# Kernel tuning notes

Measured on AMD Instinct MI355X. Metric: run time of the kernel, lower is better.

Reference implementation:

```python
import jax, jax.numpy as jnp
import numpy as np

N = 100000
E = 1600000
H = 4
C = 128
F_IN = 182
D = H * C  # 512
NEG_SLOPE = 0.2
LN_EPS = 1e-5


def _p(key, shape, scale=0.05):
    return jax.random.normal(key, shape, dtype=jnp.float32) * scale


def setup_inputs() -> dict:
    key = jax.random.key(0)
    ks = jax.random.split(key, 20)
    x = jax.random.normal(ks[0], (N, F_IN), dtype=jnp.float32)
    edge_index = jax.random.randint(ks[1], (2, E), 0, N, dtype=jnp.int64)
    inp = {
        "x": x,
        "edge_index": edge_index,
        # GAT layer 1
        "W1": _p(ks[2], (F_IN, D)),
        "a_src1": _p(ks[3], (H, C)),
        "a_dst1": _p(ks[4], (H, C)),
        "b1": _p(ks[5], (D,)),
        "g1": jnp.ones((D,), jnp.float32),
        "be1": jnp.zeros((D,), jnp.float32),
        # GAT layer 2
        "W2": _p(ks[6], (D, D)),
        "a_src2": _p(ks[7], (H, C)),
        "a_dst2": _p(ks[8], (H, C)),
        "b2": _p(ks[9], (D,)),
        "g2": jnp.ones((D,), jnp.float32),
        "be2": jnp.zeros((D,), jnp.float32),
        # classifier MLP
        "Wc1": _p(ks[10], (D, D)),
        "bc1": jnp.zeros((D,), jnp.float32),
        "Wc2": _p(ks[11], (D, 2)),
        "bc2": jnp.zeros((2,), jnp.float32),
    }
    return inp


def _gat_conv(x, src, dst, W, a_src, a_dst, b):
    # x: [N, Fin] -> h: [N, H, C]
    h = (x @ W).reshape(N, H, C)
    # per-node attention contributions: [N, H]
    s_src = jnp.sum(h * a_src, axis=-1)
    s_dst = jnp.sum(h * a_dst, axis=-1)
    # per-edge raw score: [E+N, H]
    e = jax.nn.leaky_relu(s_src[src] + s_dst[dst], NEG_SLOPE)
    # segment softmax over incoming edges of each dst node
    emax = jax.ops.segment_max(e, dst, num_segments=N)
    p = jnp.exp(e - emax[dst])
    denom = jax.ops.segment_sum(p, dst, num_segments=N)
    alpha = p / denom[dst]  # [E+N, H]
    # weighted aggregation of source features: [N, H, C]
    out = jax.ops.segment_sum(alpha[:, :, None] * h[src], dst, num_segments=N)
    return out.reshape(N, D) + b


def _layer_norm(x, g, b):
    mu = jnp.mean(x, axis=-1, keepdims=True)
    var = jnp.mean(jnp.square(x - mu), axis=-1, keepdims=True)
    return (x - mu) * jax.lax.rsqrt(var + LN_EPS) * g + b


def reference(x, edge_index, W1, a_src1, a_dst1, b1, g1, be1,
              W2, a_src2, a_dst2, b2, g2, be2, Wc1, bc1, Wc2, bc2):
    # add self-loops (PyG GATConv default)
    loops = jnp.arange(N, dtype=edge_index.dtype)
    src = jnp.concatenate([edge_index[0], loops])
    dst = jnp.concatenate([edge_index[1], loops])

    h1 = _gat_conv(x, src, dst, W1, a_src1, a_dst1, b1)
    h1 = jax.nn.elu(_layer_norm(h1, g1, be1))
    h2 = _gat_conv(h1, src, dst, W2, a_src2, a_dst2, b2)
    h2 = jax.nn.elu(_layer_norm(h2, g2, be2))
    # classifier (dropout is identity in eval)
    z = jax.nn.relu(h2 @ Wc1 + bc1)
    return z @ Wc2 + bc2
```

## Files before the change

### kernel.cpp

```cpp
#include <hip/hip_runtime.h>
#include <math.h>

static constexpr int N_NODES = 100000;
static constexpr int N_EDGES = 1600000;
static constexpr int E_TOT   = N_NODES + N_EDGES;
static constexpr int D   = 512;
static constexpr int FIN = 182;
static constexpr int K1P = 192;
static constexpr int M_PAD = 100096;
static constexpr float NEG_SLOPE = 0.2f;
static constexpr float LN_EPS = 1e-5f;

typedef __attribute__((ext_vector_type(8))) short short8;
typedef __attribute__((ext_vector_type(4))) float floatx4;
typedef __attribute__((ext_vector_type(2))) float floatx2;

__device__ __forceinline__ unsigned short f2bf(float f) {
  unsigned int x = __builtin_bit_cast(unsigned int, f);
  x += 0x7fffu + ((x >> 16) & 1u);
  return (unsigned short)(x >> 16);
}
__device__ __forceinline__ void unpack2(unsigned int w, float& lo, float& hi) {
  lo = __builtin_bit_cast(float, w << 16);
  hi = __builtin_bit_cast(float, w & 0xffff0000u);
}

typedef __attribute__((address_space(1))) const void gv_t;
typedef __attribute__((address_space(3))) void lv_t;
__device__ __forceinline__ void gll16(const void* g, void* l) {
  __builtin_amdgcn_global_load_lds((gv_t*)g, (lv_t*)l, 16, 0, 0);
}

__global__ __launch_bounds__(256) void k_init(const int* __restrict__ ei,
                                              int* __restrict__ deg,
                                              int* __restrict__ counter,
                                              int* __restrict__ flag) {
  int i = blockIdx.x * 256 + threadIdx.x;
  if (i < N_NODES) deg[i] = 0;
  if (blockIdx.x == 0) {
    bool nz = false;
#pragma unroll
    for (int rp = 0; rp < 8; ++rp) {
      int j = threadIdx.x + rp * 256;
      nz |= (ei[2 * j + 1] != 0);
    }
    __shared__ int sh[4];
    int wv = threadIdx.x >> 6;
    if ((threadIdx.x & 63) == 0) sh[wv] = 0;
    __syncthreads();
    if (__any(nz) && (threadIdx.x & 63) == 0) sh[wv] = 1;
    __syncthreads();
    if (threadIdx.x == 0) {
      *flag = sh[0] | sh[1] | sh[2] | sh[3];
      *counter = 0;
    }
  }
}

__device__ __forceinline__ int edge_src(const int* ei, int f, int i) {
  return f ? ei[i] : ei[2 * i];
}
__device__ __forceinline__ int edge_dst(const int* ei, int f, int i) {
  return f ? ei[N_EDGES + i] : ei[2 * (N_EDGES + i)];
}

__global__ __launch_bounds__(256) void k_count(const int* __restrict__ ei,
                                               const int* __restrict__ flag,
                                               int* __restrict__ deg) {
  int i = blockIdx.x * 256 + threadIdx.x;
  if (i >= E_TOT) return;
  int f = *flag;
  int d = (i < N_EDGES) ? edge_dst(ei, f, i) : (i - N_EDGES);
  atomicAdd(deg + d, 1);
}

__global__ __launch_bounds__(256) void k_alloc(const int* __restrict__ deg,
                                               int* __restrict__ off,
                                               int* __restrict__ pos,
                                               int* __restrict__ counter) {
  int i = blockIdx.x * 256 + threadIdx.x;
  if (i >= N_NODES) return;
  int r = atomicAdd(counter, deg[i]);
  off[i] = r;
  pos[i] = r;
}

__global__ __launch_bounds__(256) void k_fill(const int* __restrict__ ei,
                                              const int* __restrict__ flag,
                                              int* __restrict__ pos,
                                              int* __restrict__ csr_src) {
  int i = blockIdx.x * 256 + threadIdx.x;
  if (i >= E_TOT) return;
  int f = *flag;
  int s, d;
  if (i < N_EDGES) { s = edge_src(ei, f, i); d = edge_dst(ei, f, i); }
  else             { s = d = i - N_EDGES; }
  int slot = atomicAdd(pos + d, 1);
  csr_src[slot] = s;
}

__global__ __launch_bounds__(256) void k_cvt_x(const float* __restrict__ x,
                                               unsigned short* __restrict__ xb) {
  int i = blockIdx.x * 256 + threadIdx.x;
  if (i >= N_NODES * K1P) return;
  int row = i / K1P, col = i - row * K1P;
  float v = (col < FIN) ? x[(size_t)row * FIN + col] : 0.f;
  xb[i] = f2bf(v);
}

__global__ __launch_bounds__(256) void k_cvt_wt(const float* __restrict__ W,
                                                unsigned short* __restrict__ Wt,
                                                int K, int Kpad) {
  int i = blockIdx.x * 256 + threadIdx.x;
  if (i >= 512 * Kpad) return;
  int n = i / Kpad, k = i - n * Kpad;
  Wt[i] = f2bf(k < K ? W[(size_t)k * 512 + n] : 0.f);
}

__global__ __launch_bounds__(256) void k_out_init(const float* __restrict__ bc2,
                                                  float* __restrict__ out) {
  int i = blockIdx.x * 256 + threadIdx.x;
  if (i < N_NODES) {
    float2 v; v.x = bc2[0]; v.y = bc2[1];
    ((float2*)out)[i] = v;
  }
}

__global__ __launch_bounds__(256)
void gemm_fused(const unsigned short* __restrict__ A,
                const unsigned short* __restrict__ Bt,
                const float* __restrict__ a_src,
                const float* __restrict__ a_dst,
                float2* __restrict__ ssc,
                float* __restrict__ s_dst,
                unsigned char* __restrict__ h8,
                int lda)
{
  __shared__ unsigned short As[2][128 * 32];
  __shared__ unsigned short Bs[2][128 * 32];
  const int t    = threadIdx.x;
  const int w    = t >> 6;
  const int lane = t & 63;
  const int r    = lane & 15;
  const int q    = lane >> 4;
  const int bm   = blockIdx.y * 128;
  const int bn   = blockIdx.x * 128;
  const int wm   = (w >> 1) * 64;
  const int wn   = (w & 1) * 64;

  const int ch0 = (w * 2 + 0) * 64 + lane;
  const int ch1 = (w * 2 + 1) * 64 + lane;
  const unsigned short* gA0 = A + (size_t)(bm + (ch0 >> 2)) * lda + (ch0 & 3) * 8;
  const unsigned short* gA1 = A + (size_t)(bm + (ch1 >> 2)) * lda + (ch1 & 3) * 8;
  const unsigned short* gB0 = Bt + (size_t)(bn + (ch0 >> 2)) * lda + (ch0 & 3) * 8;
  const unsigned short* gB1 = Bt + (size_t)(bn + (ch1 >> 2)) * lda + (ch1 & 3) * 8;

  floatx4 acc[4][4] = {};

  for (int k0 = 0; k0 < lda; k0 += 64) {
    gll16(gA0 + k0,      &As[0][(w * 2 + 0) * 512]);
    gll16(gA1 + k0,      &As[0][(w * 2 + 1) * 512]);
    gll16(gB0 + k0,      &Bs[0][(w * 2 + 0) * 512]);
    gll16(gB1 + k0,      &Bs[0][(w * 2 + 1) * 512]);
    gll16(gA0 + k0 + 32, &As[1][(w * 2 + 0) * 512]);
    gll16(gA1 + k0 + 32, &As[1][(w * 2 + 1) * 512]);
    gll16(gB0 + k0 + 32, &Bs[1][(w * 2 + 0) * 512]);
    gll16(gB1 + k0 + 32, &Bs[1][(w * 2 + 1) * 512]);
    __syncthreads();

#pragma unroll
    for (int half = 0; half < 2; ++half) {
      short8 af[4], bfr[4];
#pragma unroll
      for (int im = 0; im < 4; ++im)
        af[im] = *(const short8*)(&As[half][(wm + im * 16 + r) * 32 + q * 8]);
#pragma unroll
      for (int in = 0; in < 4; ++in)
        bfr[in] = *(const short8*)(&Bs[half][(wn + in * 16 + r) * 32 + q * 8]);
#pragma unroll
      for (int im = 0; im < 4; ++im)
#pragma unroll
        for (int in = 0; in < 4; ++in)
          acc[im][in] = __builtin_amdgcn_mfma_f32_16x16x32_bf16(
              af[im], bfr[in], acc[im][in], 0, 0, 0);
    }
    __syncthreads();
  }

  float* sred = (float*)&As[0][0];
  float* qscl = (float*)&Bs[0][0];

  float asv[4], adv[4];
#pragma unroll
  for (int in = 0; in < 4; ++in) {
    asv[in] = a_src[bn + wn + in * 16 + r];
    adv[in] = a_dst[bn + wn + in * 16 + r];
  }
#pragma unroll
  for (int im = 0; im < 4; ++im) {
    float ps_[4], pd_[4], pm_[4];
#pragma unroll
    for (int rr = 0; rr < 4; ++rr) {
      float s = 0.f, d = 0.f, m = 0.f;
#pragma unroll
      for (int in = 0; in < 4; ++in) {
        float v = acc[im][in][rr];
        s += v * asv[in];
        d += v * adv[in];
        m = fmaxf(m, fabsf(v));
      }
      ps_[rr] = s; pd_[rr] = d; pm_[rr] = m;
    }
#pragma unroll
    for (int o2 = 1; o2 < 16; o2 <<= 1) {
#pragma unroll
      for (int rr = 0; rr < 4; ++rr) {
        ps_[rr] += __shfl_xor(ps_[rr], o2);
        pd_[rr] += __shfl_xor(pd_[rr], o2);
        pm_[rr] = fmaxf(pm_[rr], __shfl_xor(pm_[rr], o2));
      }
    }
    if (r == 0) {
#pragma unroll
      for (int rr = 0; rr < 4; ++rr) {
        int r64 = im * 16 + q * 4 + rr;
        sred[(w * 64 + r64) * 4 + 0] = ps_[rr];
        sred[(w * 64 + r64) * 4 + 1] = pd_[rr];
        sred[(w * 64 + r64) * 4 + 2] = pm_[rr];
      }
    }
  }
  __syncthreads();

  if (t < 128) {
    int hf = t >> 6;
    int r64 = t & 63;
    const float* pa = sred + ((hf * 2 + 0) * 64 + r64) * 4;
    const float* pb = sred + ((hf * 2 + 1) * 64 + r64) * 4;
    float s  = pa[0] + pb[0];
    float dd = pa[1] + pb[1];
    float am = fmaxf(fmaxf(pa[2], pb[2]), 1e-20f);
    qscl[t] = 127.f / am;
    int node = bm + t;
    if (node < N_NODES) {
      float2 sc; sc.x = s; sc.y = am * (1.f / 127.f);
      ssc[(size_t)node * 4 + blockIdx.x] = sc;
      s_dst[(size_t)node * 4 + blockIdx.x] = dd;
    }
  }
  __syncthreads();

#pragma unroll
  for (int im = 0; im < 4; ++im) {
#pragma unroll
    for (int rr = 0; rr < 4; ++rr) {
      int lr = wm + im * 16 + q * 4 + rr;
      float qs = qscl[lr];
      unsigned int pk = 0;
#pragma unroll
      for (int in = 0; in < 4; ++in) {
        int qv = (int)rintf(acc[im][in][rr] * qs) + 128;
        pk |= (unsigned int)(qv & 255) << (8 * in);
      }
      *(unsigned int*)(h8 + (size_t)(bm + lr) * 512 + bn + wn + 4 * r) = pk;
    }
  }
}

__global__ __launch_bounds__(256)
void gemm_cls(const unsigned short* __restrict__ A,
              const unsigned short* __restrict__ Bt,
              const float* __restrict__ bc1,
              const float* __restrict__ Wc2,
              float* __restrict__ out,
              int lda)
{
  __shared__ unsigned short As[2][128 * 32];
  __shared__ unsigned short Bs[2][128 * 32];
  const int t    = threadIdx.x;
  const int w    = t >> 6;
  const int lane = t & 63;
  const int r    = lane & 15;
  const int q    = lane >> 4;
  const int bm   = blockIdx.y * 128;
  const int bn   = blockIdx.x * 128;
  const int wm   = (w >> 1) * 64;
  const int wn   = (w & 1) * 64;

  const int ch0 = (w * 2 + 0) * 64 + lane;
  const int ch1 = (w * 2 + 1) * 64 + lane;
  const unsigned short* gA0 = A + (size_t)(bm + (ch0 >> 2)) * lda + (ch0 & 3) * 8;
  const unsigned short* gA1 = A + (size_t)(bm + (ch1 >> 2)) * lda + (ch1 & 3) * 8;
  const unsigned short* gB0 = Bt + (size_t)(bn + (ch0 >> 2)) * lda + (ch0 & 3) * 8;
  const unsigned short* gB1 = Bt + (size_t)(bn + (ch1 >> 2)) * lda + (ch1 & 3) * 8;

  floatx4 acc[4][4] = {};

  for (int k0 = 0; k0 < lda; k0 += 64) {
    gll16(gA0 + k0,      &As[0][(w * 2 + 0) * 512]);
    gll16(gA1 + k0,      &As[0][(w * 2 + 1) * 512]);
    gll16(gB0 + k0,      &Bs[0][(w * 2 + 0) * 512]);
    gll16(gB1 + k0,      &Bs[0][(w * 2 + 1) * 512]);
    gll16(gA0 + k0 + 32, &As[1][(w * 2 + 0) * 512]);
    gll16(gA1 + k0 + 32, &As[1][(w * 2 + 1) * 512]);
    gll16(gB0 + k0 + 32, &Bs[1][(w * 2 + 0) * 512]);
    gll16(gB1 + k0 + 32, &Bs[1][(w * 2 + 1) * 512]);
    __syncthreads();

#pragma unroll
    for (int half = 0; half < 2; ++half) {
      short8 af[4], bfr[4];
#pragma unroll
      for (int im = 0; im < 4; ++im)
        af[im] = *(const short8*)(&As[half][(wm + im * 16 + r) * 32 + q * 8]);
#pragma unroll
      for (int in = 0; in < 4; ++in)
        bfr[in] = *(const short8*)(&Bs[half][(wn + in * 16 + r) * 32 + q * 8]);
#pragma unroll
      for (int im = 0; im < 4; ++im)
#pragma unroll
        for (int in = 0; in < 4; ++in)
          acc[im][in] = __builtin_amdgcn_mfma_f32_16x16x32_bf16(
              af[im], bfr[in], acc[im][in], 0, 0, 0);
    }
    __syncthreads();
  }

  float p0[16], p1[16];
#pragma unroll
  for (int k = 0; k < 16; ++k) { p0[k] = 0.f; p1[k] = 0.f; }

#pragma unroll
  for (int in = 0; in < 4; ++in) {
    const int col = bn + wn + in * 16 + r;
    const float bv = bc1[col];
    const float w0 = Wc2[col * 2 + 0];
    const float w1 = Wc2[col * 2 + 1];
#pragma unroll
    for (int im = 0; im < 4; ++im)
#pragma unroll
      for (int rr = 0; rr < 4; ++rr) {
        float z = fmaxf(acc[im][in][rr] + bv, 0.f);
        p0[im * 4 + rr] += z * w0;
        p1[im * 4 + rr] += z * w1;
      }
  }
#pragma unroll
  for (int o2 = 1; o2 < 16; o2 <<= 1) {
#pragma unroll
    for (int k = 0; k < 16; ++k) {
      p0[k] += __shfl_xor(p0[k], o2);
      p1[k] += __shfl_xor(p1[k], o2);
    }
  }
  if (r == 0) {
#pragma unroll
    for (int im = 0; im < 4; ++im)
#pragma unroll
      for (int rr = 0; rr < 4; ++rr) {
        int row = bm + wm + im * 16 + q * 4 + rr;
        if (row < N_NODES) {
          atomicAdd(out + (size_t)row * 2,     p0[im * 4 + rr]);
          atomicAdd(out + (size_t)row * 2 + 1, p1[im * 4 + rr]);
        }
      }
  }
}

__global__ __launch_bounds__(256) void k_aggregate(const unsigned char* __restrict__ h8,
                                                   const float2* __restrict__ ssc,
                                                   const int* __restrict__ csr_src,
                                                   const int* __restrict__ off,
                                                   const int* __restrict__ deg,
                                                   const float* __restrict__ s_dst,
                                                   const float* __restrict__ bvec,
                                                   const float* __restrict__ gvec,
                                                   const float* __restrict__ bevec,
                                                   unsigned short* __restrict__ out) {
  int node = blockIdx.x * 4 + (threadIdx.x >> 6);
  int lane = threadIdx.x & 63;
  if (node >= N_NODES) return;
  const int o   = __builtin_amdgcn_readfirstlane(off[node]);
  const int cnt = __builtin_amdgcn_readfirstlane(deg[node]);
  const int head = lane >> 4;
  const int li   = lane & 15;
  const int cbase = head * 128 + ((li & 8) ? 64 : 0) + ((2 * li) & 15);
  const float sdH = s_dst[(size_t)node * 4 + head];

  floatx2 acc2[4] = {};
  float sumP = 0.f, sumPS = 0.f;

  int base = 0;
  if (cnt >= 16) {
    int srcl = csr_src[o + li];
    for (; base + 16 <= cnt; base += 16) {
      float2 fc = ssc[(size_t)srcl * 4 + head];
      uint2 rows[16];
#pragma unroll
      for (int j = 0; j < 16; ++j) {
        int sj = __builtin_amdgcn_readlane(srcl, j);
        rows[j] = *(const uint2*)(h8 + (size_t)sj * 512 + lane * 8);
      }
      int srcl_next = srcl;
      if (base + 32 <= cnt) srcl_next = csr_src[o + base + 16 + li];
      float e = fc.x + sdH;
      e = (e > 0.f) ? e : NEG_SLOPE * e;
      float p  = __expf(e);
      float ps = p * fc.y;
      sumP += p; sumPS += ps;
#pragma unroll
      for (int j = 0; j < 16; ++j) {
        float psj = __shfl(ps, j, 16);
        uint2 w = rows[j];
        floatx2 vp = {psj, psj};
        floatx2 b0 = {(float)( w.x        & 255u), (float)( w.y        & 255u)};
        floatx2 b1 = {(float)((w.x >>  8) & 255u), (float)((w.y >>  8) & 255u)};
        floatx2 b2 = {(float)((w.x >> 16) & 255u), (float)((w.y >> 16) & 255u)};
        floatx2 b3 = {(float)( w.x >> 24        ), (float)( w.y >> 24        )};
        acc2[0] += vp * b0;
        acc2[1] += vp * b1;
        acc2[2] += vp * b2;
        acc2[3] += vp * b3;
      }
      srcl = srcl_next;
    }
  }
  int m = cnt - base;
  if (m > 0) {
    int   idx  = (li < m) ? li : (m - 1);
    int   srcl = csr_src[o + base + idx];
    float2 fc  = ssc[(size_t)srcl * 4 + head];
    uint2 rows[16];
#pragma unroll
    for (int j = 0; j < 16; ++j) {
      if (j < m) {
        int sj = __builtin_amdgcn_readlane(srcl, j);
        rows[j] = *(const uint2*)(h8 + (size_t)sj * 512 + lane * 8);
      }
    }
    float e = fc.x + sdH;
    e = (e > 0.f) ? e : NEG_SLOPE * e;
    float p  = (li < m) ? __expf(e) : 0.f;
    float ps = p * fc.y;
    sumP += p; sumPS += ps;
#pragma unroll
    for (int j = 0; j < 16; ++j) {
      if (j < m) {
        float psj = __shfl(ps, j, 16);
        uint2 w = rows[j];
        floatx2 vp = {psj, psj};
        floatx2 b0 = {(float)( w.x        & 255u), (float)( w.y        & 255u)};
        floatx2 b1 = {(float)((w.x >>  8) & 255u), (float)((w.y >>  8) & 255u)};
        floatx2 b2 = {(float)((w.x >> 16) & 255u), (float)((w.y >> 16) & 255u)};
        floatx2 b3 = {(float)( w.x >> 24        ), (float)( w.y >> 24        )};
        acc2[0] += vp * b0;
        acc2[1] += vp * b1;
        acc2[2] += vp * b2;
        acc2[3] += vp * b3;
      }
    }
  }

#pragma unroll
  for (int o2 = 1; o2 < 16; o2 <<= 1) {
    sumP  += __shfl_xor(sumP,  o2);
    sumPS += __shfl_xor(sumPS, o2);
  }

  float acc[8];
#pragma unroll
  for (int k = 0; k < 4; ++k) { acc[k] = acc2[k].x; acc[k + 4] = acc2[k].y; }

  const float inv = 1.f / sumP;
  float bl[8];
#pragma unroll
  for (int k = 0; k < 4; ++k) {
    float2 v2 = *(const float2*)(bvec + cbase + 16 * k);
    bl[k] = v2.x; bl[k + 4] = v2.y;
  }
#pragma unroll
  for (int k = 0; k < 8; ++k)
    acc[k] = (acc[k] - 128.f * sumPS) * inv + bl[k];

  float ps2 = 0.f, pq = 0.f;
#pragma unroll
  for (int k = 0; k < 8; ++k) { ps2 += acc[k]; pq += acc[k]*acc[k]; }
#pragma unroll
  for (int o2 = 1; o2 < 64; o2 <<= 1) {
    ps2 += __shfl_xor(ps2, o2);
    pq  += __shfl_xor(pq, o2);
  }
  float mu  = ps2 * (1.f/512.f);
  float var = pq * (1.f/512.f) - mu*mu;
  float rstd = rsqrtf(var + LN_EPS);

  float gs[8], es[8];
#pragma unroll
  for (int k = 0; k < 4; ++k) {
    float2 g2 = *(const float2*)(gvec  + cbase + 16 * k);
    float2 e2 = *(const float2*)(bevec + cbase + 16 * k);
    gs[k] = g2.x; gs[k + 4] = g2.y;
    es[k] = e2.x; es[k + 4] = e2.y;
  }

  unsigned short us[8];
#pragma unroll
  for (int k = 0; k < 8; ++k) {
    float y = (acc[k] - mu) * rstd * gs[k] + es[k];
    y = (y > 0.f) ? y : expm1f(y);
    us[k] = f2bf(y);
  }
#pragma unroll
  for (int k = 0; k < 4; ++k) {
    unsigned int wv2 = (unsigned int)us[k] | ((unsigned int)us[k + 4] << 16);
    *(unsigned int*)(out + (size_t)node * D + cbase + 16 * k) = wv2;
  }
}

extern "C" void kernel_launch(void* const* d_in, const int* in_sizes, int n_in,
                              void* d_out, int out_size, void* d_ws, size_t ws_size,
                              hipStream_t stream) {
  const float* x      = (const float*)d_in[0];
  const int*   ei     = (const int*)  d_in[1];
  const float* W1     = (const float*)d_in[2];
  const float* a_src1 = (const float*)d_in[3];
  const float* a_dst1 = (const float*)d_in[4];
  const float* b1     = (const float*)d_in[5];
  const float* g1     = (const float*)d_in[6];
  const float* be1    = (const float*)d_in[7];
  const float* W2     = (const float*)d_in[8];
  const float* a_src2 = (const float*)d_in[9];
  const float* a_dst2 = (const float*)d_in[10];
  const float* b2     = (const float*)d_in[11];
  const float* g2     = (const float*)d_in[12];
  const float* be2    = (const float*)d_in[13];
  const float* Wc1    = (const float*)d_in[14];
  const float* bc1    = (const float*)d_in[15];
  const float* Wc2    = (const float*)d_in[16];
  const float* bc2    = (const float*)d_in[17];
  float* outp = (float*)d_out;

  char* p = (char*)d_ws;
  auto alloc = [&](size_t bytes) {
    char* r = p;
    p += (bytes + 255) & ~(size_t)255;
    return r;
  };
  unsigned short* obuf = (unsigned short*)alloc((size_t)M_PAD * D * 2);
  unsigned short* w1t  = (unsigned short*)alloc((size_t)512 * K1P * 2);
  unsigned short* w2t  = (unsigned short*)alloc((size_t)512 * 512 * 2);
  unsigned short* wc1t = (unsigned short*)alloc((size_t)512 * 512 * 2);
  int*   csr_src = (int*)  alloc((size_t)E_TOT * 4);
  int*   deg     = (int*)  alloc((size_t)N_NODES * 4);
  int*   off     = (int*)  alloc((size_t)N_NODES * 4);
  int*   pos     = (int*)  alloc((size_t)N_NODES * 4);
  int*   counter = (int*)  alloc(256);
  int*   flag    = (int*)  alloc(256);
  float2* ssc    = (float2*)alloc((size_t)N_NODES * 4 * 8);
  float* s_dst   = (float*)alloc((size_t)N_NODES * 4 * 4);
  unsigned char* h8 = (unsigned char*)alloc((size_t)M_PAD * 512);
  unsigned short* xb = obuf;

  const int EB = (E_TOT + 255) / 256;
  const int NB = (N_NODES + 255) / 256;
  const int NW = (N_NODES + 3) / 4;
  dim3 gg(4, M_PAD / 128);

  k_init  <<<NB, 256, 0, stream>>>(ei, deg, counter, flag);
  k_count <<<EB, 256, 0, stream>>>(ei, flag, deg);
  k_alloc <<<NB, 256, 0, stream>>>(deg, off, pos, counter);
  k_fill  <<<EB, 256, 0, stream>>>(ei, flag, pos, csr_src);

  k_cvt_x <<<(N_NODES * K1P + 255) / 256, 256, 0, stream>>>(x, xb);
  k_cvt_wt<<<(512 * K1P + 255) / 256, 256, 0, stream>>>(W1, w1t, FIN, K1P);
  k_cvt_wt<<<(512 * 512 + 255) / 256, 256, 0, stream>>>(W2, w2t, 512, 512);
  k_cvt_wt<<<(512 * 512 + 255) / 256, 256, 0, stream>>>(Wc1, wc1t, 512, 512);
  k_out_init<<<NB, 256, 0, stream>>>(bc2, outp);

  gemm_fused <<<gg, 256, 0, stream>>>(xb, w1t, a_src1, a_dst1, ssc, s_dst, h8, K1P);
  k_aggregate<<<NW, 256, 0, stream>>>(h8, ssc, csr_src, off, deg,
                                      s_dst, b1, g1, be1, obuf);

  gemm_fused <<<gg, 256, 0, stream>>>(obuf, w2t, a_src2, a_dst2, ssc, s_dst, h8, 512);
  k_aggregate<<<NW, 256, 0, stream>>>(h8, ssc, csr_src, off, deg,
                                      s_dst, b2, g2, be2, obuf);

  gemm_cls   <<<gg, 256, 0, stream>>>(obuf, wc1t, bc1, Wc2, outp, 512);
}
```

Before: 965.6 us.

## Double-buffer GEMM k-loop with prefetch and merge small setup kernels

The GEMM main loop changes from loading a 64-wide k chunk into both LDS halves and then computing, to a ping-pong scheme. The next 32-wide chunk is prefetched into the other buffer while the current one is consumed, with one barrier per step. This aims to overlap global-to-LDS loads with MFMA work. Separately, three weight-conversion launches become one 2D launch, and the output-bias init is folded into k_alloc, cutting launch overhead. Risks are more barriers per k and a possible race if the async LDS loads are not waited on properly.

After: 967.0 us. About the same (+0.1%).

```diff
diff --git a/kernel.cpp b/kernel.cpp
--- a/kernel.cpp
+++ b/kernel.cpp
@@ -31,6 +31,15 @@
   __builtin_amdgcn_global_load_lds((gv_t*)g, (lv_t*)l, 16, 0, 0);
 }
 
+__device__ __forceinline__ void stage4(const unsigned short* gA0, const unsigned short* gA1,
+                                       const unsigned short* gB0, const unsigned short* gB1,
+                                       unsigned short* As, unsigned short* Bs, int w, int k0) {
+  gll16(gA0 + k0, As + (w * 2 + 0) * 512);
+  gll16(gA1 + k0, As + (w * 2 + 1) * 512);
+  gll16(gB0 + k0, Bs + (w * 2 + 0) * 512);
+  gll16(gB1 + k0, Bs + (w * 2 + 1) * 512);
+}
+
 __global__ __launch_bounds__(256) void k_init(const int* __restrict__ ei,
                                               int* __restrict__ deg,
                                               int* __restrict__ counter,
@@ -77,12 +86,16 @@
 __global__ __launch_bounds__(256) void k_alloc(const int* __restrict__ deg,
                                                int* __restrict__ off,
                                                int* __restrict__ pos,
-                                               int* __restrict__ counter) {
+                                               int* __restrict__ counter,
+                                               const float* __restrict__ bc2,
+                                               float* __restrict__ out) {
   int i = blockIdx.x * 256 + threadIdx.x;
   if (i >= N_NODES) return;
   int r = atomicAdd(counter, deg[i]);
   off[i] = r;
   pos[i] = r;
+  float2 v; v.x = bc2[0]; v.y = bc2[1];
+  ((float2*)out)[i] = v;
 }
 
 __global__ __launch_bounds__(256) void k_fill(const int* __restrict__ ei,
@@ -108,21 +121,26 @@
   xb[i] = f2bf(v);
 }
 
-__global__ __launch_bounds__(256) void k_cvt_wt(const float* __restrict__ W,
-                                                unsigned short* __restrict__ Wt,
-                                                int K, int Kpad) {
+__global__ __launch_bounds__(256) void k_cvt_w3(const float* __restrict__ W1,
+                                                const float* __restrict__ W2,
+                                                const float* __restrict__ Wc1,
+                                                unsigned short* __restrict__ w1t,
+                                                unsigned short* __restrict__ w2t,
+                                                unsigned short* __restrict__ wc1t) {
   int i = blockIdx.x * 256 + threadIdx.x;
-  if (i >= 512 * Kpad) return;
-  int n = i / Kpad, k = i - n * Kpad;
-  Wt[i] = f2bf(k < K ? W[(size_t)k * 512 + n] : 0.f);
-}
-
-__global__ __launch_bounds__(256) void k_out_init(const float* __restrict__ bc2,
-                                                  float* __restrict__ out) {
-  int i = blockIdx.x * 256 + threadIdx.x;
-  if (i < N_NODES) {
-    float2 v; v.x = bc2[0]; v.y = bc2[1];
-    ((float2*)out)[i] = v;
+  int which = blockIdx.y;
+  if (which == 0) {
+    if (i >= 512 * K1P) return;
+    int n = i / K1P, k = i - n * K1P;
+    w1t[i] = f2bf(k < FIN ? W1[(size_t)k * 512 + n] : 0.f);
+  } else if (which == 1) {
+    if (i >= 512 * 512) return;
+    int n = i >> 9, k = i & 511;
+    w2t[i] = f2bf(W2[(size_t)k * 512 + n]);
+  } else {
+    if (i >= 512 * 512) return;
+    int n = i >> 9, k = i & 511;
+    wc1t[i] = f2bf(Wc1[(size_t)k * 512 + n]);
   }
 }
 
@@ -157,35 +175,28 @@
 
   floatx4 acc[4][4] = {};
 
-  for (int k0 = 0; k0 < lda; k0 += 64) {
-    gll16(gA0 + k0,      &As[0][(w * 2 + 0) * 512]);
-    gll16(gA1 + k0,      &As[0][(w * 2 + 1) * 512]);
-    gll16(gB0 + k0,      &Bs[0][(w * 2 + 0) * 512]);
-    gll16(gB1 + k0,      &Bs[0][(w * 2 + 1) * 512]);
-    gll16(gA0 + k0 + 32, &As[1][(w * 2 + 0) * 512]);
-    gll16(gA1 + k0 + 32, &As[1][(w * 2 + 1) * 512]);
-    gll16(gB0 + k0 + 32, &Bs[1][(w * 2 + 0) * 512]);
-    gll16(gB1 + k0 + 32, &Bs[1][(w * 2 + 1) * 512]);
+  int cur = 0;
+  stage4(gA0, gA1, gB0, gB1, &As[0][0], &Bs[0][0], w, 0);
+  for (int k0 = 0; k0 < lda; k0 += 32) {
     __syncthreads();
-
-#pragma unroll
-    for (int half = 0; half < 2; ++half) {
-      short8 af[4], bfr[4];
-#pragma unroll
-      for (int im = 0; im < 4; ++im)
-        af[im] = *(const short8*)(&As[half][(wm + im * 16 + r) * 32 + q * 8]);
+    if (k0 + 32 < lda)
+      stage4(gA0, gA1, gB0, gB1, &As[cur ^ 1][0], &Bs[cur ^ 1][0], w, k0 + 32);
+    short8 af[4], bfr[4];
+#pragma unroll
+    for (int im = 0; im < 4; ++im)
+      af[im] = *(const short8*)(&As[cur][(wm + im * 16 + r) * 32 + q * 8]);
+#pragma unroll
+    for (int in = 0; in < 4; ++in)
+      bfr[in] = *(const short8*)(&Bs[cur][(wn + in * 16 + r) * 32 + q * 8]);
+#pragma unroll
+    for (int im = 0; im < 4; ++im)
 #pragma unroll
       for (int in = 0; in < 4; ++in)
-        bfr[in] = *(const short8*)(&Bs[half][(wn + in * 16 + r) * 32 + q * 8]);
-#pragma unroll
-      for (int im = 0; im < 4; ++im)
-#pragma unroll
-        for (int in = 0; in < 4; ++in)
-          acc[im][in] = __builtin_amdgcn_mfma_f32_16x16x32_bf16(
-              af[im], bfr[in], acc[im][in], 0, 0, 0);
-    }
-    __syncthreads();
-  }
+        acc[im][in] = __builtin_amdgcn_mfma_f32_16x16x32_bf16(
+            af[im], bfr[in], acc[im][in], 0, 0, 0);
+    cur ^= 1;
+  }
+  __syncthreads();
 
   float* sred = (float*)&As[0][0];
   float* qscl = (float*)&Bs[0][0];
@@ -296,34 +307,26 @@
 
   floatx4 acc[4][4] = {};
 
-  for (int k0 = 0; k0 < lda; k0 += 64) {
-    gll16(gA0 + k0,      &As[0][(w * 2 + 0) * 512]);
-    gll16(gA1 + k0,      &As[0][(w * 2 + 1) * 512]);
-    gll16(gB0 + k0,      &Bs[0][(w * 2 + 0) * 512]);
-    gll16(gB1 + k0,      &Bs[0][(w * 2 + 1) * 512]);
-    gll16(gA0 + k0 + 32, &As[1][(w * 2 + 0) * 512]);
-    gll16(gA1 + k0 + 32, &As[1][(w * 2 + 1) * 512]);
-    gll16(gB0 + k0 + 32, &Bs[1][(w * 2 + 0) * 512]);
-    gll16(gB1 + k0 + 32, &Bs[1][(w * 2 + 1) * 512]);
+  int cur = 0;
+  stage4(gA0, gA1, gB0, gB1, &As[0][0], &Bs[0][0], w, 0);
+  for (int k0 = 0; k0 < lda; k0 += 32) {
     __syncthreads();
-
-#pragma unroll
-    for (int half = 0; half < 2; ++half) {
-      short8 af[4], bfr[4];
-#pragma unroll
-      for (int im = 0; im < 4; ++im)
-        af[im] = *(const short8*)(&As[half][(wm + im * 16 + r) * 32 + q * 8]);
+    if (k0 + 32 < lda)
+      stage4(gA0, gA1, gB0, gB1, &As[cur ^ 1][0], &Bs[cur ^ 1][0], w, k0 + 32);
+    short8 af[4], bfr[4];
+#pragma unroll
+    for (int im = 0; im < 4; ++im)
+      af[im] = *(const short8*)(&As[cur][(wm + im * 16 + r) * 32 + q * 8]);
+#pragma unroll
+    for (int in = 0; in < 4; ++in)
+      bfr[in] = *(const short8*)(&Bs[cur][(wn + in * 16 + r) * 32 + q * 8]);
+#pragma unroll
+    for (int im = 0; im < 4; ++im)
 #pragma unroll
       for (int in = 0; in < 4; ++in)
-        bfr[in] = *(const short8*)(&Bs[half][(wn + in * 16 + r) * 32 + q * 8]);
-#pragma unroll
-      for (int im = 0; im < 4; ++im)
-#pragma unroll
-        for (int in = 0; in < 4; ++in)
-          acc[im][in] = __builtin_amdgcn_mfma_f32_16x16x32_bf16(
-              af[im], bfr[in], acc[im][in], 0, 0, 0);
-    }
-    __syncthreads();
+        acc[im][in] = __builtin_amdgcn_mfma_f32_16x16x32_bf16(
+            af[im], bfr[in], acc[im][in], 0, 0, 0);
+    cur ^= 1;
   }
 
   float p0[16], p1[16];
@@ -568,14 +571,11 @@
 
   k_init  <<<NB, 256, 0, stream>>>(ei, deg, counter, flag);
   k_count <<<EB, 256, 0, stream>>>(ei, flag, deg);
-  k_alloc <<<NB, 256, 0, stream>>>(deg, off, pos, counter);
+  k_alloc <<<NB, 256, 0, stream>>>(deg, off, pos, counter, bc2, outp);
   k_fill  <<<EB, 256, 0, stream>>>(ei, flag, pos, csr_src);
 
   k_cvt_x <<<(N_NODES * K1P + 255) / 256, 256, 0, stream>>>(x, xb);
-  k_cvt_wt<<<(512 * K1P + 255) / 256, 256, 0, stream>>>(W1, w1t, FIN, K1P);
-  k_cvt_wt<<<(512 * 512 + 255) / 256, 256, 0, stream>>>(W2, w2t, 512, 512);
-  k_cvt_wt<<<(512 * 512 + 255) / 256, 256, 0, stream>>>(Wc1, wc1t, 512, 512);
-  k_out_init<<<NB, 256, 0, stream>>>(bc2, outp);
+  k_cvt_w3<<<dim3(1024, 3), 256, 0, stream>>>(W1, W2, Wc1, w1t, w2t, wc1t);
 
   gemm_fused <<<gg, 256, 0, stream>>>(xb, w1t, a_src1, a_dst1, ssc, s_dst, h8, K1P);
   k_aggregate<<<NW, 256, 0, stream>>>(h8, ssc, csr_src, off, deg,
```
